# Kernel tuning notes

Hardware: AMD Instinct MI355X
Metric: run time of the kernel (lower is better)

Reference implementation:

```python
import jax, jax.numpy as jnp
import numpy as np

N_NODES = 20000
N_EDGES = 320000
IN_CH = 512
HID = 128
HEADS = 4
OUT_CH = 30
NEG_SLOPE = 0.2  # PyG GATConv default negative_slope


def add_self_loops(ei, n):
    loops = jnp.arange(n, dtype=ei.dtype)
    return jnp.concatenate([ei, jnp.stack([loops, loops])], axis=1)


def gat_layer(x, ei, W, a_src, a_dst, b, concat):
    # x: [N, F_in], ei: [2, E] (source row 0 -> target row 1), W: [F_in, H*C]
    n = x.shape[0]
    H, C = a_src.shape
    h = (x @ W).reshape(n, H, C)                      # [N, H, C]
    src, dst = ei[0], ei[1]
    al_src = jnp.einsum('nhc,hc->nh', h, a_src)       # [N, H]
    al_dst = jnp.einsum('nhc,hc->nh', h, a_dst)
    e = al_src[src] + al_dst[dst]                     # [E, H]
    e = jnp.where(e > 0, e, NEG_SLOPE * e)            # LeakyReLU
    # segment softmax over destination nodes (stable)
    emax = jax.lax.stop_gradient(jax.ops.segment_max(e, dst, num_segments=n))
    p = jnp.exp(e - emax[dst])
    denom = jax.ops.segment_sum(p, dst, num_segments=n)
    alpha = p / denom[dst]                            # [E, H]
    msg = h[src] * alpha[:, :, None]                  # [E, H, C]
    out = jax.ops.segment_sum(msg, dst, num_segments=n)  # [N, H, C]
    out = out.reshape(n, H * C) if concat else out.mean(axis=1)
    return out + b


def setup_inputs() -> dict:
    key = jax.random.key(0)
    ks = jax.random.split(key, 12)
    s = 0.05
    x = jax.random.normal(ks[0], (N_NODES, IN_CH), jnp.float32)
    edge_index = jax.random.randint(ks[1], (2, N_EDGES), 0, N_NODES, jnp.int32)
    return {
        'x': x,
        'edge_index': edge_index,
        'W1': jax.random.normal(ks[2], (IN_CH, HEADS * HID), jnp.float32) * s,
        'a_src1': jax.random.normal(ks[3], (HEADS, HID), jnp.float32) * s,
        'a_dst1': jax.random.normal(ks[4], (HEADS, HID), jnp.float32) * s,
        'b1': jnp.zeros((HEADS * HID,), jnp.float32),
        'W2': jax.random.normal(ks[5], (HEADS * HID, OUT_CH), jnp.float32) * s,
        'a_src2': jax.random.normal(ks[6], (1, OUT_CH), jnp.float32) * s,
        'a_dst2': jax.random.normal(ks[7], (1, OUT_CH), jnp.float32) * s,
        'b2': jnp.zeros((OUT_CH,), jnp.float32),
        'Wd': jax.random.normal(ks[8], (OUT_CH, IN_CH), jnp.float32) * s,
        'bd': jnp.zeros((IN_CH,), jnp.float32),
    }


def reference(x, edge_index, W1, a_src1, a_dst1, b1, W2, a_src2, a_dst2, b2, Wd, bd):
    n = x.shape[0]
    ei = add_self_loops(edge_index, n)
    h = gat_layer(x, ei, W1, a_src1, a_dst1, b1, concat=True)   # [N, HEADS*HID]
    h = jax.nn.elu(h)                                           # dropout is identity in eval
    z = gat_layer(h, ei, W2, a_src2, a_dst2, b2, concat=False)  # [N, OUT_CH]
    x_hat = z @ Wd + bd                                         # [N, IN_CH]
    return (x_hat, z)
```

## Files before the change

### kernel.cpp

```cpp
#include <hip/hip_runtime.h>
#include <hip/hip_bf16.h>
#include <stdint.h>

#define N_NODES 20000
#define N_EDGES 320000
#define IN_CH 512
#define HID 128
#define HEADS 4
#define HC 512
#define OUT_CH 30
#define NEG_SLOPE 0.2f
#define M_PAD 20096

typedef _Float16 half8 __attribute__((ext_vector_type(8)));
typedef _Float16 half4v __attribute__((ext_vector_type(4)));
typedef _Float16 half2v __attribute__((ext_vector_type(2)));
typedef float f32x4 __attribute__((ext_vector_type(4)));

static __device__ __forceinline__ float lrelu(float e) { return e > 0.f ? e : NEG_SLOPE * e; }

static __device__ __forceinline__ void gload16(const void* gsrc, void* ldst) {
  __builtin_amdgcn_global_load_lds(
      (const __attribute__((address_space(1))) uint32_t*)gsrc,
      (__attribute__((address_space(3))) uint32_t*)ldst,
      16, 0, 0);
}

__global__ __launch_bounds__(256) void k_cast_x(const float* __restrict__ x,
                                                _Float16* __restrict__ xh) {
  int i = blockIdx.x * blockDim.x + threadIdx.x;
  int base = i * 4;
  int row = base >> 9;
  half4v o;
  if (row < N_NODES) {
    float4 v = *(const float4*)(x + (size_t)base);
    o[0] = (_Float16)v.x; o[1] = (_Float16)v.y; o[2] = (_Float16)v.z; o[3] = (_Float16)v.w;
  } else {
    o[0] = o[1] = o[2] = o[3] = (_Float16)0.f;
  }
  *(half4v*)(xh + (size_t)base) = o;
}

__global__ __launch_bounds__(256) void k_cast_w1t(const float* __restrict__ W1,
                                                  _Float16* __restrict__ W1t) {
  __shared__ float t[64][65];
  const int bk = blockIdx.x * 64;
  const int bn = blockIdx.y * 64;
  const int tid = threadIdx.x;
#pragma unroll
  for (int it = 0; it < 16; it++) {
    int idx = tid + it * 256;
    int r = idx >> 6, c = idx & 63;
    t[r][c] = W1[(size_t)(bk + r) * HC + bn + c];
  }
  __syncthreads();
#pragma unroll
  for (int it = 0; it < 16; it++) {
    int idx = tid + it * 256;
    int rn = idx >> 6, ck = idx & 63;
    W1t[(size_t)(bn + rn) * IN_CH + bk + ck] = (_Float16)t[ck][rn];
  }
}

__global__ __launch_bounds__(256) void k_cast_w2t(const float* __restrict__ W2,
                                                  _Float16* __restrict__ w2t) {
  int idx = blockIdx.x * blockDim.x + threadIdx.x;
  if (idx >= 32 * 512) return;
  int n = idx >> 9, k = idx & 511;
  w2t[idx] = (n < OUT_CH) ? (_Float16)W2[(size_t)k * OUT_CH + n] : (_Float16)0.f;
}

__global__ __launch_bounds__(256) void k_gemm1_mfma(const _Float16* __restrict__ A,
                                                    const _Float16* __restrict__ Bt,
                                                    _Float16* __restrict__ C) {
  __shared__ _Float16 smem[128 * 136];
  _Float16* As = smem;
  _Float16* Bs = smem + 128 * 64;
  _Float16* Cs = smem;
  const int tid = threadIdx.x;
  const int lane = tid & 63;
  const int w = tid >> 6;
  const int bm = blockIdx.x * 128;
  const int bn = blockIdx.y * 128;

  const int lrow = lane >> 3;
  const int schunk = (lane & 7) ^ lrow;

  const int wm = w >> 1, wn = w & 1;
  const int r15 = lane & 15;
  const int q = lane >> 4;
  const int a_row0 = wm * 64 + r15;
  const int b_row0 = wn * 64 + r15;

  f32x4 acc[4][4];
  const f32x4 zero = {0.f, 0.f, 0.f, 0.f};
#pragma unroll
  for (int i = 0; i < 4; i++)
#pragma unroll
    for (int j = 0; j < 4; j++) acc[i][j] = zero;

  for (int kb = 0; kb < 8; kb++) {
    const int kof = kb * 64 + schunk * 8;
#pragma unroll
    for (int t = 0; t < 4; t++) {
      const int row = w * 32 + t * 8;
      gload16(A + (size_t)(bm + row + lrow) * IN_CH + kof, (void*)(As + row * 64));
      gload16(Bt + (size_t)(bn + row + lrow) * IN_CH + kof, (void*)(Bs + row * 64));
    }
    __syncthreads();
#pragma unroll
    for (int s = 0; s < 2; s++) {
      const int cs = ((s * 4 + q) ^ (lane & 7)) * 8;
      half8 af[4], bf[4];
#pragma unroll
      for (int i = 0; i < 4; i++) af[i] = *(const half8*)&As[(a_row0 + i * 16) * 64 + cs];
#pragma unroll
      for (int j = 0; j < 4; j++) bf[j] = *(const half8*)&Bs[(b_row0 + j * 16) * 64 + cs];
#pragma unroll
      for (int i = 0; i < 4; i++)
#pragma unroll
        for (int j = 0; j < 4; j++)
          acc[i][j] = __builtin_amdgcn_mfma_f32_16x16x32_f16(af[i], bf[j], acc[i][j], 0, 0, 0);
    }
    __syncthreads();
  }
#pragma unroll
  for (int i = 0; i < 4; i++)
#pragma unroll
    for (int j = 0; j < 4; j++)
#pragma unroll
      for (int r = 0; r < 4; r++) {
        const int row = wm * 64 + i * 16 + q * 4 + r;
        const int col = wn * 64 + j * 16 + r15;
        Cs[row * 136 + col] = (_Float16)acc[i][j][r];
      }
  __syncthreads();
#pragma unroll
  for (int it = 0; it < 8; it++) {
    int cidx = tid + it * 256;
    int row = cidx >> 4, c16 = cidx & 15;
    int gm = bm + row;
    if (gm < N_NODES)
      *(half8*)(C + (size_t)gm * HC + bn + c16 * 8) = *(const half8*)&Cs[row * 136 + c16 * 8];
  }
}

__global__ __launch_bounds__(256) void k_al1(const _Float16* __restrict__ h,
                                             const float* __restrict__ a_src,
                                             const float* __restrict__ a_dst,
                                             float* __restrict__ al_s,
                                             float* __restrict__ al_d) {
  const int lane = threadIdx.x & 63;
  const int wid = (blockIdx.x * 256 + threadIdx.x) >> 6;
  const int c0 = lane * 8;
  float as[8], ad[8];
#pragma unroll
  for (int j = 0; j < 8; j++) {
    as[j] = a_src[c0 + j];
    ad[j] = a_dst[c0 + j];
  }
  for (int n = wid; n < N_NODES; n += 1024) {
    half8 hv = *(const half8*)(h + (size_t)n * HC + c0);
    float s = 0.f, d = 0.f;
#pragma unroll
    for (int j = 0; j < 8; j++) {
      float hf = (float)hv[j];
      s += hf * as[j];
      d += hf * ad[j];
    }
#pragma unroll
    for (int off = 8; off; off >>= 1) {
      s += __shfl_down(s, off);
      d += __shfl_down(d, off);
    }
    if ((lane & 15) == 0) {
      al_s[n * HEADS + (lane >> 4)] = s;
      al_d[n * HEADS + (lane >> 4)] = d;
    }
  }
}

#define PARTS 79
__global__ void k_count(const int* __restrict__ dst, int* __restrict__ cnt) {
  int e = blockIdx.x * blockDim.x + threadIdx.x;
  if (e < N_EDGES) atomicAdd(&cnt[dst[e]], 1);
}
__global__ __launch_bounds__(256) void k_scan_part(const int* __restrict__ cnt,
                                                   int* __restrict__ part) {
  __shared__ int ws[4];
  int i = blockIdx.x * 256 + threadIdx.x;
  int v = (i < N_NODES) ? cnt[i] : 0;
  int lane = threadIdx.x & 63;
#pragma unroll
  for (int off = 32; off; off >>= 1) v += __shfl_down(v, off);
  if (lane == 0) ws[threadIdx.x >> 6] = v;
  __syncthreads();
  if (threadIdx.x == 0) part[blockIdx.x] = ws[0] + ws[1] + ws[2] + ws[3];
}
__global__ __launch_bounds__(128) void k_scan_tops(int* __restrict__ part,
                                                   int* __restrict__ offs) {
  __shared__ int buf[128];
  int t = threadIdx.x;
  int v = (t < PARTS) ? part[t] : 0;
  buf[t] = v;
  __syncthreads();
#pragma unroll
  for (int off = 1; off < 128; off <<= 1) {
    int x = (t >= off) ? buf[t - off] : 0;
    __syncthreads();
    buf[t] += x;
    __syncthreads();
  }
  if (t < PARTS) part[t] = buf[t] - v;
  if (t == PARTS - 1) offs[N_NODES] = buf[t];
}
__global__ __launch_bounds__(256) void k_scan_final(const int* __restrict__ cnt,
                                                    const int* __restrict__ part,
                                                    int* __restrict__ offs,
                                                    int* __restrict__ cursor) {
  __shared__ int buf[256];
  int i = blockIdx.x * 256 + threadIdx.x;
  int t = threadIdx.x;
  int v = (i < N_NODES) ? cnt[i] : 0;
  buf[t] = v;
  __syncthreads();
#pragma unroll
  for (int off = 1; off < 256; off <<= 1) {
    int x = (t >= off) ? buf[t - off] : 0;
    __syncthreads();
    buf[t] += x;
    __syncthreads();
  }
  if (i < N_NODES) {
    int ex = part[blockIdx.x] + buf[t] - v;
    offs[i] = ex;
    cursor[i] = ex;
  }
}
__global__ void k_scatter(const int* __restrict__ src, const int* __restrict__ dst,
                          int* __restrict__ cursor, int* __restrict__ srcs) {
  int e = blockIdx.x * blockDim.x + threadIdx.x;
  if (e < N_EDGES) {
    int pos = atomicAdd(&cursor[dst[e]], 1);
    srcs[pos] = src[e];
  }
}

__global__ __launch_bounds__(256) void k_agg1(const _Float16* __restrict__ h,
                                              const float* __restrict__ al_s,
                                              const float* __restrict__ al_d,
                                              const int* __restrict__ offs,
                                              const int* __restrict__ srcs,
                                              const float* __restrict__ b1,
                                              _Float16* __restrict__ hm) {
  __shared__ int2 s_sp[4][64];
  const int wv = threadIdx.x >> 6;
  const int lane = threadIdx.x & 63;
  const int qq = lane >> 4;
  const int l16 = lane & 15;
  const int head = blockIdx.x / 1250;
  const int n = (blockIdx.x % 1250) * 16 + wv * 4 + qq;
  const int cb = head * HID + l16 * 8;

  const float adn = al_d[n * HEADS + head];
  const float pself = __expf(lrelu(al_s[n * HEADS + head] + adn));

  half8 hv = *(const half8*)(h + (size_t)n * HC + cb);
  float acc[8];
  float den = pself;
#pragma unroll
  for (int j = 0; j < 8; j++) acc[j] = pself * (float)hv[j];

  const int beg = offs[n];
  const int cnt = offs[n + 1] - beg;
  int mx = cnt;
  mx = max(mx, __shfl_xor(mx, 16));
  mx = max(mx, __shfl_xor(mx, 32));

  for (int base = 0; base < mx; base += 16) {
    int s = n;
    float p = 0.f;
    if (base + l16 < cnt) {
      s = srcs[beg + base + l16];
      p = __expf(lrelu(al_s[s * HEADS + head] + adn));
    }
    s_sp[wv][lane] = make_int2(s, __float_as_int(p));
    __builtin_amdgcn_wave_barrier();
    const int m = min(16, cnt - base);
    for (int k = 0; k < m; k++) {
      int2 sp = s_sp[wv][qq * 16 + k];
      float pk = __int_as_float(sp.y);
      half8 v = *(const half8*)(h + (size_t)sp.x * HC + cb);
      den += pk;
#pragma unroll
      for (int j = 0; j < 8; j++) acc[j] += pk * (float)v[j];
    }
    __builtin_amdgcn_wave_barrier();
  }
  const float inv = 1.f / den;
  float4 bb0 = *(const float4*)(b1 + cb);
  float4 bb1 = *(const float4*)(b1 + cb + 4);
  float ob[8] = {bb0.x, bb0.y, bb0.z, bb0.w, bb1.x, bb1.y, bb1.z, bb1.w};
  half8 ov;
#pragma unroll
  for (int j = 0; j < 8; j++) {
    float o = acc[j] * inv + ob[j];
    o = o > 0.f ? o : __expf(o) - 1.f;
    ov[j] = (_Float16)o;
  }
  *(half8*)(hm + (size_t)n * HC + cb) = ov;
}

__global__ __launch_bounds__(256) void k_gemm2_mfma(const _Float16* __restrict__ hm,
                                                    const _Float16* __restrict__ w2t,
                                                    const float* __restrict__ a_s2,
                                                    const float* __restrict__ a_d2,
                                                    float* __restrict__ zpre,
                                                    float* __restrict__ al_s2,
                                                    float* __restrict__ al_d2) {
  __shared__ _Float16 Bs[32 * 520];
  __shared__ _Float16 As[64 * 136];
  const int tid = threadIdx.x;
  const int lane = tid & 63;
  const int w = tid >> 6;
  const int bm = blockIdx.x * 64;
  const int n15 = lane & 15;
  const int q = lane >> 4;

#pragma unroll
  for (int it = 0; it < 8; it++) {
    int idx = (tid + it * 256) * 8;
    int n = idx >> 9, k = idx & 511;
    *(half8*)&Bs[n * 520 + k] = *(const half8*)(w2t + idx);
  }

  f32x4 acc0 = {0.f, 0.f, 0.f, 0.f}, acc1 = {0.f, 0.f, 0.f, 0.f};
  for (int kt = 0; kt < HC; kt += 128) {
#pragma unroll
    for (int p = 0; p < 4; p++) {
      int row = (tid >> 4) + p * 16;
      int kof = (tid & 15) * 8;
      int gm = bm + row;
      half8 v = {};
      if (gm < N_NODES) v = *(const half8*)(hm + (size_t)gm * HC + kt + kof);
      *(half8*)&As[row * 136 + kof] = v;
    }
    __syncthreads();
#pragma unroll
    for (int ks = 0; ks < 128; ks += 32) {
      half8 af = *(const half8*)&As[(w * 16 + n15) * 136 + ks + q * 8];
      half8 b0 = *(const half8*)&Bs[n15 * 520 + kt + ks + q * 8];
      half8 b1 = *(const half8*)&Bs[(16 + n15) * 520 + kt + ks + q * 8];
      acc0 = __builtin_amdgcn_mfma_f32_16x16x32_f16(af, b0, acc0, 0, 0, 0);
      acc1 = __builtin_amdgcn_mfma_f32_16x16x32_f16(af, b1, acc1, 0, 0, 0);
    }
    __syncthreads();
  }
  const float asn0 = (n15 < OUT_CH) ? a_s2[n15] : 0.f;
  const float asn1 = (n15 + 16 < OUT_CH) ? a_s2[n15 + 16] : 0.f;
  const float adn0 = (n15 < OUT_CH) ? a_d2[n15] : 0.f;
  const float adn1 = (n15 + 16 < OUT_CH) ? a_d2[n15 + 16] : 0.f;
#pragma unroll
  for (int r = 0; r < 4; r++) {
    const int gm = bm + w * 16 + q * 4 + r;
    const bool ok = gm < N_NODES;
    if (ok) {
      zpre[(size_t)gm * OUT_CH + n15] = acc0[r];
      if (n15 + 16 < OUT_CH) zpre[(size_t)gm * OUT_CH + n15 + 16] = acc1[r];
    }
    float s = acc0[r] * asn0 + acc1[r] * asn1;
    float d = acc0[r] * adn0 + acc1[r] * adn1;
#pragma unroll
    for (int off = 8; off; off >>= 1) {
      s += __shfl_xor(s, off);
      d += __shfl_xor(d, off);
    }
    if (n15 == 0 && ok) {
      al_s2[gm] = s;
      al_d2[gm] = d;
    }
  }
}

__global__ __launch_bounds__(256) void k_agg2(const float* __restrict__ zpre,
                                              const float* __restrict__ al_s2,
                                              const float* __restrict__ al_d2,
                                              const int* __restrict__ offs,
                                              const int* __restrict__ srcs,
                                              const float* __restrict__ b2,
                                              float* __restrict__ zout) {
  __shared__ int2 s_sp[4][64];
  const int wv = threadIdx.x >> 6;
  const int lane = threadIdx.x & 63;
  const int hh = lane >> 5;
  const int l32 = lane & 31;
  const int n = blockIdx.x * 8 + wv * 2 + hh;
  const float ad2n = al_d2[n];
  const float pself = __expf(lrelu(al_s2[n] + ad2n));
  const bool act = l32 < OUT_CH;
  float zv = act ? zpre[(size_t)n * OUT_CH + l32] : 0.f;
  float acc = pself * zv;
  float den = pself;

  const int beg = offs[n];
  const int cnt = offs[n + 1] - beg;
  int mx = max(cnt, __shfl_xor(cnt, 32));

  for (int base = 0; base < mx; base += 32) {
    int s = n;
    float p = 0.f;
    if (base + l32 < cnt) {
      s = srcs[beg + base + l32];
      p = __expf(lrelu(al_s2[s] + ad2n));
    }
    s_sp[wv][lane] = make_int2(s, __float_as_int(p));
    __builtin_amdgcn_wave_barrier();
    const int m = min(32, cnt - base);
    for (int k = 0; k < m; k++) {
      int2 sp = s_sp[wv][hh * 32 + k];
      float pk = __int_as_float(sp.y);
      float sv = act ? zpre[(size_t)sp.x * OUT_CH + l32] : 0.f;
      den += pk;
      acc += pk * sv;
    }
    __builtin_amdgcn_wave_barrier();
  }
  if (act) zout[(size_t)n * OUT_CH + l32] = acc / den + b2[l32];
}

__global__ __launch_bounds__(256) void k_dec(const float* __restrict__ z,
                                             const float* __restrict__ Wd,
                                             const float* __restrict__ bd,
                                             float* __restrict__ xhat) {
  __shared__ float zs[64][32];
  const int tid = threadIdx.x;
  const int c = blockIdx.y * 256 + tid;
  float wd[32];
#pragma unroll
  for (int k = 0; k < OUT_CH; k++) wd[k] = Wd[(size_t)k * IN_CH + c];
  wd[30] = wd[31] = 0.f;
  const int n0 = blockIdx.x * 64;
  for (int idx = tid; idx < 64 * 32; idx += 256) {
    int r = idx >> 5, cc = idx & 31;
    int row = n0 + r;
    zs[r][cc] = (cc < OUT_CH && row < N_NODES) ? z[(size_t)row * OUT_CH + cc] : 0.f;
  }
  __syncthreads();
  const float b0 = bd[c];
  for (int i = 0; i < 64; i++) {
    int row = n0 + i;
    if (row >= N_NODES) break;
    float a0 = b0;
#pragma unroll
    for (int k4 = 0; k4 < 8; k4++) {
      float4 zv = *(const float4*)&zs[i][k4 * 4];
      a0 += zv.x * wd[k4 * 4 + 0] + zv.y * wd[k4 * 4 + 1] +
            zv.z * wd[k4 * 4 + 2] + zv.w * wd[k4 * 4 + 3];
    }
    xhat[(size_t)row * IN_CH + c] = a0;
  }
}

extern "C" void kernel_launch(void* const* d_in, const int* in_sizes, int n_in,
                              void* d_out, int out_size, void* d_ws, size_t ws_size,
                              hipStream_t stream) {
  const float* x    = (const float*)d_in[0];
  const int*   ei   = (const int*)d_in[1];
  const float* W1   = (const float*)d_in[2];
  const float* a_s1 = (const float*)d_in[3];
  const float* a_d1 = (const float*)d_in[4];
  const float* b1   = (const float*)d_in[5];
  const float* W2   = (const float*)d_in[6];
  const float* a_s2 = (const float*)d_in[7];
  const float* a_d2 = (const float*)d_in[8];
  const float* b2   = (const float*)d_in[9];
  const float* Wd   = (const float*)d_in[10];
  const float* bd   = (const float*)d_in[11];

  float* xhat = (float*)d_out;
  float* zout = xhat + (size_t)N_NODES * IN_CH;

  const int* srcv = ei;
  const int* dstv = ei + N_EDGES;

  char* w = (char*)d_ws;
  auto alloc = [&](size_t bytes) {
    void* p = (void*)w;
    w += (bytes + 255) & ~(size_t)255;
    return p;
  };
  _Float16* xh   = (_Float16*)alloc((size_t)M_PAD * IN_CH * 2);
  _Float16* w1t  = (_Float16*)alloc((size_t)HC * IN_CH * 2);
  _Float16* w2t  = (_Float16*)alloc((size_t)32 * HC * 2);
  _Float16* h    = (_Float16*)alloc((size_t)N_NODES * HC * 2);
  _Float16* hm   = (_Float16*)alloc((size_t)N_NODES * HC * 2);
  float* zpre  = (float*)alloc((size_t)N_NODES * OUT_CH * 4);
  float* al_s1v= (float*)alloc((size_t)N_NODES * HEADS * 4);
  float* al_d1v= (float*)alloc((size_t)N_NODES * HEADS * 4);
  float* al_s2v= (float*)alloc((size_t)N_NODES * 4);
  float* al_d2v= (float*)alloc((size_t)N_NODES * 4);
  int*   cnt   = (int*)alloc((size_t)N_NODES * 4);
  int*   offs  = (int*)alloc((size_t)(N_NODES + 1) * 4);
  int*   cursor= (int*)alloc((size_t)N_NODES * 4);
  int*   srcs  = (int*)alloc((size_t)N_EDGES * 4);
  int*   part  = (int*)alloc((size_t)PARTS * 4);

  const int EB = (N_EDGES + 255) / 256;

  k_cast_x<<<(M_PAD * IN_CH / 4 + 255) / 256, 256, 0, stream>>>(x, xh);
  k_cast_w1t<<<dim3(IN_CH / 64, HC / 64), 256, 0, stream>>>(W1, w1t);
  k_cast_w2t<<<(32 * HC + 255) / 256, 256, 0, stream>>>(W2, w2t);
  k_gemm1_mfma<<<dim3(M_PAD / 128, HC / 128), 256, 0, stream>>>(xh, w1t, h);
  k_al1<<<256, 256, 0, stream>>>(h, a_s1, a_d1, al_s1v, al_d1v);
  hipMemsetAsync(cnt, 0, (size_t)N_NODES * 4, stream);
  k_count<<<EB, 256, 0, stream>>>(dstv, cnt);
  k_scan_part<<<PARTS, 256, 0, stream>>>(cnt, part);
  k_scan_tops<<<1, 128, 0, stream>>>(part, offs);
  k_scan_final<<<PARTS, 256, 0, stream>>>(cnt, part, offs, cursor);
  k_scatter<<<EB, 256, 0, stream>>>(srcv, dstv, cursor, srcs);
  k_agg1<<<1250 * HEADS, 256, 0, stream>>>(h, al_s1v, al_d1v, offs, srcs, b1, hm);
  k_gemm2_mfma<<<(N_NODES + 63) / 64, 256, 0, stream>>>(hm, w2t, a_s2, a_d2, zpre,
                                                        al_s2v, al_d2v);
  k_agg2<<<N_NODES / 8, 256, 0, stream>>>(zpre, al_s2v, al_d2v, offs, srcs, b2, zout);
  k_dec<<<dim3((N_NODES + 63) / 64, 2), 256, 0, stream>>>(zout, Wd, bd, xhat);
}
```

Before: 278.9 us.

## Fuse attention logits into GEMM epilogue, merge prep kernels, use shuffles in aggregation

Computes the layer-1 attention logits inside the GEMM1 epilogue from the tile already staged in shared memory, so the separate k_al1 pass over h disappears. The two weight cast kernels are merged into one launch, and the memset of the count array is folded into the x cast kernel. Both aggregation kernels now broadcast source indices and weights by wave shuffles instead of LDS. They also unroll the neighbour gather by four to keep more loads in flight. The cost is padded iterations when a neighbour count is not a multiple of four, and these rely on the padded lanes carrying zero weight.

```diff
diff --git a/kernel.cpp b/kernel.cpp
--- a/kernel.cpp
+++ b/kernel.cpp
@@ -14,7 +14,6 @@
 
 typedef _Float16 half8 __attribute__((ext_vector_type(8)));
 typedef _Float16 half4v __attribute__((ext_vector_type(4)));
-typedef _Float16 half2v __attribute__((ext_vector_type(2)));
 typedef float f32x4 __attribute__((ext_vector_type(4)));
 
 static __device__ __forceinline__ float lrelu(float e) { return e > 0.f ? e : NEG_SLOPE * e; }
@@ -27,8 +26,10 @@
 }
 
 __global__ __launch_bounds__(256) void k_cast_x(const float* __restrict__ x,
-                                                _Float16* __restrict__ xh) {
+                                                _Float16* __restrict__ xh,
+                                                int* __restrict__ cnt) {
   int i = blockIdx.x * blockDim.x + threadIdx.x;
+  if (i < N_NODES) cnt[i] = 0;
   int base = i * 4;
   int row = base >> 9;
   half4v o;
@@ -41,38 +42,43 @@
   *(half4v*)(xh + (size_t)base) = o;
 }
 
-__global__ __launch_bounds__(256) void k_cast_w1t(const float* __restrict__ W1,
-                                                  _Float16* __restrict__ W1t) {
+__global__ __launch_bounds__(256) void k_prep_w(const float* __restrict__ W1,
+                                                const float* __restrict__ W2,
+                                                _Float16* __restrict__ W1t,
+                                                _Float16* __restrict__ w2t) {
   __shared__ float t[64][65];
-  const int bk = blockIdx.x * 64;
-  const int bn = blockIdx.y * 64;
+  const int b = blockIdx.x;
   const int tid = threadIdx.x;
-#pragma unroll
-  for (int it = 0; it < 16; it++) {
-    int idx = tid + it * 256;
-    int r = idx >> 6, c = idx & 63;
-    t[r][c] = W1[(size_t)(bk + r) * HC + bn + c];
-  }
-  __syncthreads();
-#pragma unroll
-  for (int it = 0; it < 16; it++) {
-    int idx = tid + it * 256;
-    int rn = idx >> 6, ck = idx & 63;
-    W1t[(size_t)(bn + rn) * IN_CH + bk + ck] = (_Float16)t[ck][rn];
-  }
-}
-
-__global__ __launch_bounds__(256) void k_cast_w2t(const float* __restrict__ W2,
-                                                  _Float16* __restrict__ w2t) {
-  int idx = blockIdx.x * blockDim.x + threadIdx.x;
-  if (idx >= 32 * 512) return;
-  int n = idx >> 9, k = idx & 511;
-  w2t[idx] = (n < OUT_CH) ? (_Float16)W2[(size_t)k * OUT_CH + n] : (_Float16)0.f;
+  if (b < 64) {
+    const int bk = (b & 7) * 64;
+    const int bn = (b >> 3) * 64;
+#pragma unroll
+    for (int it = 0; it < 16; it++) {
+      int idx = tid + it * 256;
+      int r = idx >> 6, c = idx & 63;
+      t[r][c] = W1[(size_t)(bk + r) * HC + bn + c];
+    }
+    __syncthreads();
+#pragma unroll
+    for (int it = 0; it < 16; it++) {
+      int idx = tid + it * 256;
+      int rn = idx >> 6, ck = idx & 63;
+      W1t[(size_t)(bn + rn) * IN_CH + bk + ck] = (_Float16)t[ck][rn];
+    }
+  } else {
+    int idx = (b - 64) * 256 + tid;
+    int n = idx >> 9, k = idx & 511;
+    w2t[idx] = (n < OUT_CH) ? (_Float16)W2[(size_t)k * OUT_CH + n] : (_Float16)0.f;
+  }
 }
 
 __global__ __launch_bounds__(256) void k_gemm1_mfma(const _Float16* __restrict__ A,
                                                     const _Float16* __restrict__ Bt,
-                                                    _Float16* __restrict__ C) {
+                                                    _Float16* __restrict__ C,
+                                                    const float* __restrict__ a_src,
+                                                    const float* __restrict__ a_dst,
+                                                    float* __restrict__ al_s,
+                                                    float* __restrict__ al_d) {
   __shared__ _Float16 smem[128 * 136];
   _Float16* As = smem;
   _Float16* Bs = smem + 128 * 64;
@@ -143,40 +149,32 @@
     if (gm < N_NODES)
       *(half8*)(C + (size_t)gm * HC + bn + c16 * 8) = *(const half8*)&Cs[row * 136 + c16 * 8];
   }
-}
-
-__global__ __launch_bounds__(256) void k_al1(const _Float16* __restrict__ h,
-                                             const float* __restrict__ a_src,
-                                             const float* __restrict__ a_dst,
-                                             float* __restrict__ al_s,
-                                             float* __restrict__ al_d) {
-  const int lane = threadIdx.x & 63;
-  const int wid = (blockIdx.x * 256 + threadIdx.x) >> 6;
-  const int c0 = lane * 8;
-  float as[8], ad[8];
-#pragma unroll
-  for (int j = 0; j < 8; j++) {
-    as[j] = a_src[c0 + j];
-    ad[j] = a_dst[c0 + j];
-  }
-  for (int n = wid; n < N_NODES; n += 1024) {
-    half8 hv = *(const half8*)(h + (size_t)n * HC + c0);
-    float s = 0.f, d = 0.f;
-#pragma unroll
-    for (int j = 0; j < 8; j++) {
-      float hf = (float)hv[j];
-      s += hf * as[j];
-      d += hf * ad[j];
-    }
-#pragma unroll
-    for (int off = 8; off; off >>= 1) {
-      s += __shfl_down(s, off);
-      d += __shfl_down(d, off);
-    }
-    if ((lane & 15) == 0) {
-      al_s[n * HEADS + (lane >> 4)] = s;
-      al_d[n * HEADS + (lane >> 4)] = d;
-    }
+  const int head = blockIdx.y;
+  const int row = tid >> 1;
+  const int hf = tid & 1;
+  const float* asp = a_src + head * HID + hf * 64;
+  const float* adp = a_dst + head * HID + hf * 64;
+  float s = 0.f, d = 0.f;
+#pragma unroll
+  for (int j8 = 0; j8 < 8; j8++) {
+    half8 cv = *(const half8*)&Cs[row * 136 + hf * 64 + j8 * 8];
+    float4 a0 = *(const float4*)(asp + j8 * 8);
+    float4 a1 = *(const float4*)(asp + j8 * 8 + 4);
+    float4 d0 = *(const float4*)(adp + j8 * 8);
+    float4 d1 = *(const float4*)(adp + j8 * 8 + 4);
+    float c0 = (float)cv[0], c1 = (float)cv[1], c2 = (float)cv[2], c3 = (float)cv[3];
+    float c4 = (float)cv[4], c5 = (float)cv[5], c6 = (float)cv[6], c7 = (float)cv[7];
+    s += c0 * a0.x + c1 * a0.y + c2 * a0.z + c3 * a0.w +
+         c4 * a1.x + c5 * a1.y + c6 * a1.z + c7 * a1.w;
+    d += c0 * d0.x + c1 * d0.y + c2 * d0.z + c3 * d0.w +
+         c4 * d1.x + c5 * d1.y + c6 * d1.z + c7 * d1.w;
+  }
+  s += __shfl_xor(s, 1);
+  d += __shfl_xor(d, 1);
+  const int gm = bm + row;
+  if (hf == 0 && gm < N_NODES) {
+    al_s[gm * HEADS + head] = s;
+    al_d[gm * HEADS + head] = d;
   }
 }
 
@@ -253,13 +251,11 @@
                                               const int* __restrict__ srcs,
                                               const float* __restrict__ b1,
                                               _Float16* __restrict__ hm) {
-  __shared__ int2 s_sp[4][64];
-  const int wv = threadIdx.x >> 6;
   const int lane = threadIdx.x & 63;
   const int qq = lane >> 4;
   const int l16 = lane & 15;
   const int head = blockIdx.x / 1250;
-  const int n = (blockIdx.x % 1250) * 16 + wv * 4 + qq;
+  const int n = (blockIdx.x % 1250) * 16 + (threadIdx.x >> 6) * 4 + qq;
   const int cb = head * HID + l16 * 8;
 
   const float adn = al_d[n * HEADS + head];
@@ -276,26 +272,36 @@
   int mx = cnt;
   mx = max(mx, __shfl_xor(mx, 16));
   mx = max(mx, __shfl_xor(mx, 32));
+  const int kb = qq * 16;
 
   for (int base = 0; base < mx; base += 16) {
-    int s = n;
-    float p = 0.f;
+    int sreg = n;
+    float preg = 0.f;
     if (base + l16 < cnt) {
-      s = srcs[beg + base + l16];
-      p = __expf(lrelu(al_s[s * HEADS + head] + adn));
-    }
-    s_sp[wv][lane] = make_int2(s, __float_as_int(p));
-    __builtin_amdgcn_wave_barrier();
-    const int m = min(16, cnt - base);
-    for (int k = 0; k < m; k++) {
-      int2 sp = s_sp[wv][qq * 16 + k];
-      float pk = __int_as_float(sp.y);
-      half8 v = *(const half8*)(h + (size_t)sp.x * HC + cb);
-      den += pk;
-#pragma unroll
-      for (int j = 0; j < 8; j++) acc[j] += pk * (float)v[j];
-    }
-    __builtin_amdgcn_wave_barrier();
+      sreg = srcs[beg + base + l16];
+      preg = __expf(lrelu(al_s[sreg * HEADS + head] + adn));
+    }
+    int m = min(16, cnt - base);
+    int m4 = (m + 3) & ~3;
+    for (int k = 0; k < m4; k += 4) {
+      int s0 = __shfl(sreg, kb + k);
+      int s1 = __shfl(sreg, kb + k + 1);
+      int s2 = __shfl(sreg, kb + k + 2);
+      int s3 = __shfl(sreg, kb + k + 3);
+      float p0 = __shfl(preg, kb + k);
+      float p1 = __shfl(preg, kb + k + 1);
+      float p2 = __shfl(preg, kb + k + 2);
+      float p3 = __shfl(preg, kb + k + 3);
+      half8 v0 = *(const half8*)(h + (size_t)s0 * HC + cb);
+      half8 v1 = *(const half8*)(h + (size_t)s1 * HC + cb);
+      half8 v2 = *(const half8*)(h + (size_t)s2 * HC + cb);
+      half8 v3 = *(const half8*)(h + (size_t)s3 * HC + cb);
+      den += p0 + p1 + p2 + p3;
+#pragma unroll
+      for (int j = 0; j < 8; j++)
+        acc[j] += p0 * (float)v0[j] + p1 * (float)v1[j] +
+                  p2 * (float)v2[j] + p3 * (float)v3[j];
+    }
   }
   const float inv = 1.f / den;
   float4 bb0 = *(const float4*)(b1 + cb);
@@ -389,12 +395,10 @@
                                               const int* __restrict__ srcs,
                                               const float* __restrict__ b2,
                                               float* __restrict__ zout) {
-  __shared__ int2 s_sp[4][64];
-  const int wv = threadIdx.x >> 6;
   const int lane = threadIdx.x & 63;
   const int hh = lane >> 5;
   const int l32 = lane & 31;
-  const int n = blockIdx.x * 8 + wv * 2 + hh;
+  const int n = blockIdx.x * 8 + (threadIdx.x >> 6) * 2 + hh;
   const float ad2n = al_d2[n];
   const float pself = __expf(lrelu(al_s2[n] + ad2n));
   const bool act = l32 < OUT_CH;
@@ -405,25 +409,33 @@
   const int beg = offs[n];
   const int cnt = offs[n + 1] - beg;
   int mx = max(cnt, __shfl_xor(cnt, 32));
+  const int kb = hh * 32;
 
   for (int base = 0; base < mx; base += 32) {
-    int s = n;
-    float p = 0.f;
+    int sreg = n;
+    float preg = 0.f;
     if (base + l32 < cnt) {
-      s = srcs[beg + base + l32];
-      p = __expf(lrelu(al_s2[s] + ad2n));
-    }
-    s_sp[wv][lane] = make_int2(s, __float_as_int(p));
-    __builtin_amdgcn_wave_barrier();
-    const int m = min(32, cnt - base);
-    for (int k = 0; k < m; k++) {
-      int2 sp = s_sp[wv][hh * 32 + k];
-      float pk = __int_as_float(sp.y);
-      float sv = act ? zpre[(size_t)sp.x * OUT_CH + l32] : 0.f;
-      den += pk;
-      acc += pk * sv;
-    }
-    __builtin_amdgcn_wave_barrier();
+      sreg = srcs[beg + base + l32];
+      preg = __expf(lrelu(al_s2[sreg] + ad2n));
+    }
+    int m = min(32, cnt - base);
+    int m4 = (m + 3) & ~3;
+    for (int k = 0; k < m4; k += 4) {
+      int s0 = __shfl(sreg, kb + k);
+      int s1 = __shfl(sreg, kb + k + 1);
+      int s2 = __shfl(sreg, kb + k + 2);
+      int s3 = __shfl(sreg, kb + k + 3);
+      float p0 = __shfl(preg, kb + k);
+      float p1 = __shfl(preg, kb + k + 1);
+      float p2 = __shfl(preg, kb + k + 2);
+      float p3 = __shfl(preg, kb + k + 3);
+      float v0 = act ? zpre[(size_t)s0 * OUT_CH + l32] : 0.f;
+      float v1 = act ? zpre[(size_t)s1 * OUT_CH + l32] : 0.f;
+      float v2 = act ? zpre[(size_t)s2 * OUT_CH + l32] : 0.f;
+      float v3 = act ? zpre[(size_t)s3 * OUT_CH + l32] : 0.f;
+      den += p0 + p1 + p2 + p3;
+      acc += p0 * v0 + p1 * v1 + p2 * v2 + p3 * v3;
+    }
   }
   if (act) zout[(size_t)n * OUT_CH + l32] = acc / den + b2[l32];
 }
@@ -507,12 +519,10 @@
 
   const int EB = (N_EDGES + 255) / 256;
 
-  k_cast_x<<<(M_PAD * IN_CH / 4 + 255) / 256, 256, 0, stream>>>(x, xh);
-  k_cast_w1t<<<dim3(IN_CH / 64, HC / 64), 256, 0, stream>>>(W1, w1t);
-  k_cast_w2t<<<(32 * HC + 255) / 256, 256, 0, stream>>>(W2, w2t);
-  k_gemm1_mfma<<<dim3(M_PAD / 128, HC / 128), 256, 0, stream>>>(xh, w1t, h);
-  k_al1<<<256, 256, 0, stream>>>(h, a_s1, a_d1, al_s1v, al_d1v);
-  hipMemsetAsync(cnt, 0, (size_t)N_NODES * 4, stream);
+  k_prep_w<<<128, 256, 0, stream>>>(W1, W2, w1t, w2t);
+  k_cast_x<<<M_PAD * IN_CH / 4 / 256, 256, 0, stream>>>(x, xh, cnt);
+  k_gemm1_mfma<<<dim3(M_PAD / 128, HC / 128), 256, 0, stream>>>(xh, w1t, h, a_s1, a_d1,
+                                                                al_s1v, al_d1v);
   k_count<<<EB, 256, 0, stream>>>(dstv, cnt);
   k_scan_part<<<PARTS, 256, 0, stream>>>(cnt, part);
   k_scan_tops<<<1, 128, 0, stream>>>(part, offs);
```

New measurement: 267.0 us. -4.3%, faster.
